# Optimization experiments

Hardware: AMD Instinct MI355X
Metric: run time of the kernel (lower is better)

The kernel has to match this reference:

```python
import jax, jax.numpy as jnp
from jax import lax
import numpy as np

D_MODEL = 96; D_STATE = 16; SSM_RATIO = 2.0; D_CONV = 3; K = 4
D_INNER = int(SSM_RATIO * D_MODEL)      # 192
DT_RANK = -(-D_MODEL // 16)             # ceil(96/16) = 6
B_SZ = 4; H = 32; W = 32

# ---- zig-zag (snake) index helpers (static numpy) ----
def _snake_h(Hh, Ww):
    idx = np.tile(np.arange(Ww), (Hh, 1)); idx[1::2] = idx[1::2, ::-1]; return idx  # (H,W)

def _snake_v(Hh, Ww):
    idx = np.tile(np.arange(Hh)[:, None], (1, Ww)); idx[:, 1::2] = idx[::-1, 1::2]; return idx  # (H,W)

def _h_scan(x, d):
    Hh, Ww = x.shape[-2:]
    if d == 'left':
        x = jnp.flip(x, (-1, -2))
    return x[:, :, np.arange(Hh)[:, None], _snake_h(Hh, Ww)]

def _v_scan(x, d):
    Bb, Cc, Hh, Ww = x.shape
    if d == 'up':
        x = jnp.flip(x, (-1, -2))
    t = x[:, :, _snake_v(Hh, Ww), np.arange(Ww)[None, :]]  # gather along H per column
    return jnp.swapaxes(t, -1, -2).reshape(Bb, Cc, Hh, Ww)

def _h_merge(x, d):
    Hh, Ww = x.shape[-2:]
    t = x[:, :, np.arange(Hh)[:, None], _snake_h(Hh, Ww)]
    if d == 'left':
        t = jnp.flip(t, (-1, -2))
    return t

def _v_merge(x, d):
    Hh, Ww = x.shape[-2:]
    t2 = jnp.swapaxes(x, -1, -2)  # (B,C,W,H); requires H==W like the torch source
    t = t2[:, :, _snake_v(Hh, Ww), np.arange(Ww)[None, :]]
    if d == 'up':
        t = jnp.flip(t, (-1, -2))
    return t

def cross_scan(x):
    return jnp.stack([_v_scan(x, 'down'), _v_scan(x, 'up'), _h_scan(x, 'right'), _h_scan(x, 'left')], axis=1)

def cross_merge(ys):
    return (_v_merge(ys[:, 0], 'down') + _v_merge(ys[:, 1], 'up')
            + _h_merge(ys[:, 2], 'right') + _h_merge(ys[:, 3], 'left'))

def selective_scan(u, delta, A, Bs, Cs, Dp, delta_bias):
    # u,delta:(B,K,D,L)  A:(K,D,N)  Bs,Cs:(B,K,N,L)  Dp,delta_bias:(K,D)
    delta = jax.nn.softplus(delta + delta_bias[None, :, :, None])
    dA = jnp.exp(jnp.einsum('bkdl,kdn->lbkdn', delta, A))
    dBu = jnp.einsum('bkdl,bkdl,bknl->lbkdn', delta, u, Bs)
    Ct = jnp.moveaxis(Cs, -1, 0)  # (L,B,K,N)
    def step(h, inp):
        dA_t, dBu_t, c_t = inp
        h = dA_t * h + dBu_t
        return h, jnp.einsum('bkdn,bkn->bkd', h, c_t)
    h0 = jnp.zeros(dA.shape[1:], u.dtype)
    _, ys = lax.scan(step, h0, (dA, dBu, Ct))
    return jnp.moveaxis(ys, 0, -1) + Dp[None, :, :, None] * u  # (B,K,D,L)

def setup_inputs() -> dict:
    key = jax.random.key(0)
    ks = jax.random.split(key, 8)
    x = jax.random.normal(ks[0], (B_SZ, D_MODEL, H, W), jnp.float32)
    in_proj_w = jax.random.normal(ks[1], (2 * D_INNER, D_MODEL), jnp.float32) * (D_MODEL ** -0.5)
    conv_w = jax.random.normal(ks[2], (D_INNER, 1, D_CONV, D_CONV), jnp.float32) * 0.2  # depthwise
    conv_b = jnp.zeros((D_INNER,), jnp.float32)
    x_proj_w = jax.random.normal(ks[3], (K, DT_RANK + 2 * D_STATE, D_INNER), jnp.float32) * (D_INNER ** -0.5)
    s = DT_RANK ** -0.5
    dt_w = jax.random.uniform(ks[4], (K, D_INNER, DT_RANK), jnp.float32, -s, s)
    dt = jax.random.uniform(ks[5], (K, D_INNER), jnp.float32, 0.001, 0.1)
    dt_b = jnp.log(jnp.expm1(dt))  # inverse softplus, as in dt_init
    A_logs = jnp.tile(jnp.log(jnp.arange(1, D_STATE + 1, dtype=jnp.float32)), (K * D_INNER, 1))
    Ds = jnp.ones((K * D_INNER,), jnp.float32)
    gn_gamma = jnp.ones((D_INNER,), jnp.float32)
    gn_beta = jnp.zeros((D_INNER,), jnp.float32)
    out_proj_w = jax.random.normal(ks[6], (D_MODEL, D_INNER), jnp.float32) * (D_INNER ** -0.5)
    return {'x': x, 'in_proj_w': in_proj_w, 'conv_w': conv_w, 'conv_b': conv_b,
            'x_proj_w': x_proj_w, 'dt_w': dt_w, 'dt_b': dt_b, 'A_logs': A_logs, 'Ds': Ds,
            'gn_gamma': gn_gamma, 'gn_beta': gn_beta, 'out_proj_w': out_proj_w}

def reference(x, in_proj_w, conv_w, conv_b, x_proj_w, dt_w, dt_b, A_logs, Ds, gn_gamma, gn_beta, out_proj_w):
    Bb, _, Hh, Ww = x.shape; L = Hh * Ww
    xz = jnp.einsum('bchw,oc->bohw', x, in_proj_w)          # in_proj (1x1 conv, no bias)
    xx, z = jnp.split(xz, 2, axis=1)
    z = jax.nn.silu(z)
    xx = lax.conv_general_dilated(xx, conv_w, (1, 1), 'SAME', feature_group_count=D_INNER,
                                  dimension_numbers=('NCHW', 'OIHW', 'NCHW')) + conv_b[None, :, None, None]
    xx = jax.nn.silu(xx)
    xs = cross_scan(xx).reshape(Bb, K, D_INNER, L)          # 4-direction zig-zag scan
    x_dbl = jnp.einsum('bkdl,kcd->bkcl', xs, x_proj_w)
    dts = jnp.einsum('bkrl,kdr->bkdl', x_dbl[:, :, :DT_RANK], dt_w)
    Bs = x_dbl[:, :, DT_RANK:DT_RANK + D_STATE]
    Cs = x_dbl[:, :, DT_RANK + D_STATE:]
    A = -jnp.exp(A_logs).reshape(K, D_INNER, D_STATE)
    y = selective_scan(xs, dts, A, Bs, Cs, Ds.reshape(K, D_INNER), dt_b)
    y = cross_merge(y.reshape(Bb, K, D_INNER, Hh, Ww))       # (B,D,H,W)
    # out_norm: GroupNorm(1, d_inner) == layernorm over (C,H,W) per sample
    mu = jnp.mean(y, axis=(1, 2, 3), keepdims=True)
    var = jnp.var(y, axis=(1, 2, 3), keepdims=True)
    y = (y - mu) * lax.rsqrt(var + 1e-6)
    y = y * gn_gamma[None, :, None, None] + gn_beta[None, :, None, None]
    y = y * z
    return jnp.einsum('bchw,oc->bohw', y, out_proj_w)
```

## Files before the change

### kernel.cpp

```cpp
#include <hip/hip_runtime.h>
#include <math.h>

#define Bsz 4
#define DM 96
#define DI 192
#define NS 16
#define RK 6
#define KK 4
#define HH 32
#define WW 32
#define LL 1024
#define NC 64
#define CS 16

__device__ __forceinline__ float silu_f(float x) { return x / (1.f + __expf(-x)); }

__device__ __forceinline__ int l_of_hw(int k, int h, int w) {
    if (k == 1 || k == 3) { h = 31 - h; w = 31 - w; }
    if (k < 2) return w * 32 + ((w & 1) ? 31 - h : h);
    return h * 32 + ((h & 1) ? 31 - w : w);
}

__global__ void in_proj_k(const float* __restrict__ x, const float* __restrict__ w,
                          float* __restrict__ xx, float* __restrict__ zs,
                          float* __restrict__ stats) {
    int bi = blockIdx.x;
    int t = threadIdx.x;
    if (bi == 0 && t < 2 * Bsz) stats[t] = 0.f;
    int lb = bi & 3;
    int og = (bi >> 2) % 48;
    int b = bi / 192;
    int l = lb * 256 + t;
    const float* xb = x + (size_t)b * DM * LL + l;
    float acc[8];
#pragma unroll
    for (int g = 0; g < 8; g++) acc[g] = 0.f;
    for (int c = 0; c < DM; c++) {
        float xv = xb[(size_t)c * LL];
#pragma unroll
        for (int g = 0; g < 8; g++)
            acc[g] = fmaf(xv, w[(size_t)(og * 8 + g) * DM + c], acc[g]);
    }
#pragma unroll
    for (int g = 0; g < 8; g++) {
        int o = og * 8 + g;
        if (o < DI) xx[((size_t)b * DI + o) * LL + l] = acc[g];
        else        zs[((size_t)b * DI + (o - DI)) * LL + l] = silu_f(acc[g]);
    }
}

__global__ void convxs_k(const float* __restrict__ xx, const float* __restrict__ cw,
                         const float* __restrict__ cb, float* __restrict__ xs) {
    __shared__ float tile[32][65];
    int bi = blockIdx.x;
    int h0 = bi % 32;
    int dt = (bi / 32) % 3;
    int b = bi / 96;
    int d0 = dt * 64;
    int t = threadIdx.x;
    int wi = t & 31, dg = t >> 5;

#pragma unroll
    for (int pass = 0; pass < 8; pass++) {
        int di = pass * 8 + dg;
        int d = d0 + di;
        const float* xp = xx + ((size_t)b * DI + d) * LL;
        const float* wp = cw + d * 9;
        float acc = cb[d];
#pragma unroll
        for (int kh = 0; kh < 3; kh++) {
            int hh = h0 + kh - 1;
            if (hh < 0 || hh >= HH) continue;
#pragma unroll
            for (int kw = 0; kw < 3; kw++) {
                int ww2 = wi + kw - 1;
                if (ww2 < 0 || ww2 >= WW) continue;
                acc = fmaf(xp[hh * WW + ww2], wp[kh * 3 + kw], acc);
            }
        }
        tile[wi][di] = silu_f(acc);
    }
    __syncthreads();

    int di = t & 63, hg = t >> 6;
#pragma unroll
    for (int k = 0; k < KK; k++) {
        float* xsk = xs + ((size_t)b * KK + k) * LL * DI;
#pragma unroll
        for (int rep = 0; rep < 8; rep++) {
            int w2 = rep * 4 + hg;
            int l = l_of_hw(k, h0, w2);
            xsk[(size_t)l * DI + d0 + di] = tile[w2][di];
        }
    }
}

__global__ void __launch_bounds__(512)
xdbl_k(const float* __restrict__ xs, const float* __restrict__ xpw,
       float* __restrict__ xdbl) {
    __shared__ float tile[64 * 193];
    int blk = blockIdx.x;
    int bk = blk >> 4, lt = blk & 15;
    int k = bk & 3;
    int t = threadIdx.x;

    const float4* src4 = (const float4*)(xs + ((size_t)bk * LL + lt * 64) * DI);
#pragma unroll
    for (int i = 0; i < 6; i++) {
        int j4 = t + i * 512;
        float4 v = src4[j4];
        int l = j4 / 48;
        int d = (j4 % 48) * 4;
        float* dst = &tile[l * 193 + d];
        dst[0] = v.x; dst[1] = v.y; dst[2] = v.z; dst[3] = v.w;
    }
    __syncthreads();

    int ll = t & 63;
    int cg = t >> 6;
    int c0 = cg * 5;
    int wlim = (c0 + 5 <= 38) ? 5 : (38 - c0);
    const float* wk = xpw + (size_t)k * 38 * DI;

    float acc[5];
#pragma unroll
    for (int j = 0; j < 5; j++) acc[j] = 0.f;
    const float* xrow = &tile[ll * 193];
#pragma unroll 4
    for (int d = 0; d < DI; d++) {
        float xv = xrow[d];
#pragma unroll
        for (int j = 0; j < 5; j++) {
            int cc = c0 + j; cc = (cc > 37) ? 37 : cc;
            acc[j] = fmaf(xv, wk[(size_t)cc * DI + d], acc[j]);
        }
    }
    float* orow = xdbl + ((size_t)bk * LL + lt * 64 + ll) * 38;
#pragma unroll
    for (int j = 0; j < 5; j++)
        if (j < wlim) orow[c0 + j] = acc[j];
}

__global__ void scan_p1(const float* __restrict__ xs, const float* __restrict__ xdbl,
                        const float* __restrict__ dtw_g, const float* __restrict__ dtb_g,
                        const float* __restrict__ Alog,
                        float* __restrict__ Pst, float* __restrict__ Hloc) {
    int blk = blockIdx.x;
    int bk = blk / NC, c = blk % NC;
    int k = bk & 3;
    int d = threadIdx.x;
    int kd = k * DI + d;

    float A[NS];
#pragma unroll
    for (int n = 0; n < NS; n++) A[n] = -__expf(Alog[(size_t)kd * NS + n]);
    float dtw[RK];
#pragma unroll
    for (int r = 0; r < RK; r++) dtw[r] = dtw_g[(size_t)kd * RK + r];
    float dtb = dtb_g[kd];

    float h[NS], P[NS];
#pragma unroll
    for (int n = 0; n < NS; n++) { h[n] = 0.f; P[n] = 1.f; }

    const float* xdbase = xdbl + ((size_t)bk * LL + c * CS) * 38;
    const float* xsbase = xs + ((size_t)bk * LL + c * CS) * DI;

    for (int s = 0; s < CS; s++) {
        const float* xd = xdbase + s * 38;
        float dt = dtb;
#pragma unroll
        for (int r = 0; r < RK; r++) dt = fmaf(xd[r], dtw[r], dt);
        dt = (dt > 20.f) ? dt : log1pf(__expf(dt));
        float du = dt * xsbase[(size_t)s * DI + d];
#pragma unroll
        for (int n = 0; n < NS; n++) {
            float a = __expf(dt * A[n]);
            h[n] = fmaf(a, h[n], du * xd[6 + n]);
            P[n] *= a;
        }
    }
    size_t base = ((size_t)blk * DI + d) * NS;
#pragma unroll
    for (int n = 0; n < NS; n++) { Pst[base + n] = P[n]; Hloc[base + n] = h[n]; }
}

__global__ void scan_mid(const float* __restrict__ Pst, float* __restrict__ Hloc) {
    int gid = blockIdx.x * 256 + threadIdx.x;
    int bk = gid / (DI * NS);
    int dn = gid % (DI * NS);
    size_t base = (size_t)bk * NC * DI * NS + dn;
    float h = 0.f;
    for (int c = 0; c < NC; c++) {
        size_t a = base + (size_t)c * DI * NS;
        float p = Pst[a];
        float loc = Hloc[a];
        Hloc[a] = h;
        h = fmaf(p, h, loc);
    }
}

__global__ void scan_p3(const float* __restrict__ xs, const float* __restrict__ xdbl,
                        const float* __restrict__ dtw_g, const float* __restrict__ dtb_g,
                        const float* __restrict__ Alog, const float* __restrict__ Ds,
                        const float* __restrict__ Hin, float* __restrict__ ys) {
    int blk = blockIdx.x;
    int bk = blk / NC, c = blk % NC;
    int k = bk & 3;
    int d = threadIdx.x;
    int kd = k * DI + d;

    float A[NS];
#pragma unroll
    for (int n = 0; n < NS; n++) A[n] = -__expf(Alog[(size_t)kd * NS + n]);
    float dtw[RK];
#pragma unroll
    for (int r = 0; r < RK; r++) dtw[r] = dtw_g[(size_t)kd * RK + r];
    float dtb = dtb_g[kd];
    float Dp = Ds[kd];

    float h[NS];
    size_t hbase = ((size_t)blk * DI + d) * NS;
#pragma unroll
    for (int n = 0; n < NS; n++) h[n] = Hin[hbase + n];

    const float* xdbase = xdbl + ((size_t)bk * LL + c * CS) * 38;
    const float* xsbase = xs + ((size_t)bk * LL + c * CS) * DI;
    float* ybase = ys + ((size_t)bk * LL + c * CS) * DI;

    for (int s = 0; s < CS; s++) {
        const float* xd = xdbase + s * 38;
        float dt = dtb;
#pragma unroll
        for (int r = 0; r < RK; r++) dt = fmaf(xd[r], dtw[r], dt);
        dt = (dt > 20.f) ? dt : log1pf(__expf(dt));
        float u = xsbase[(size_t)s * DI + d];
        float du = dt * u;
        float y = 0.f;
#pragma unroll
        for (int n = 0; n < NS; n++) {
            float a = __expf(dt * A[n]);
            h[n] = fmaf(a, h[n], du * xd[6 + n]);
            y = fmaf(h[n], xd[22 + n], y);
        }
        ybase[(size_t)s * DI + d] = fmaf(Dp, u, y);
    }
}

#define MT 16
__global__ void merge_k(const float* __restrict__ ys, float* __restrict__ ym,
                        float* __restrict__ stats) {
    __shared__ float tile[MT][DI + 1];
    __shared__ float sh1[3], sh2[3];
    int b = blockIdx.y;
    int hw0 = blockIdx.x * MT;
    int d = threadIdx.x;
    const float* yb = ys + (size_t)b * KK * LL * DI;

    float s1 = 0.f, s2 = 0.f;
#pragma unroll
    for (int hwi = 0; hwi < MT; hwi++) {
        int hw = hw0 + hwi;
        int h = hw >> 5, w = hw & 31;
        int l0 = l_of_hw(0, h, w);
        int l1 = l_of_hw(1, h, w);
        int l2 = l_of_hw(2, h, w);
        int l3 = l_of_hw(3, h, w);
        float v = yb[((size_t)0 * LL + l0) * DI + d]
                + yb[((size_t)1 * LL + l1) * DI + d]
                + yb[((size_t)2 * LL + l2) * DI + d]
                + yb[((size_t)3 * LL + l3) * DI + d];
        tile[hwi][d] = v;
        s1 += v; s2 = fmaf(v, v, s2);
    }
#pragma unroll
    for (int off = 32; off > 0; off >>= 1) {
        s1 += __shfl_down(s1, off);
        s2 += __shfl_down(s2, off);
    }
    int lane = threadIdx.x & 63, wid = threadIdx.x >> 6;
    if (lane == 0) { sh1[wid] = s1; sh2[wid] = s2; }
    __syncthreads();
    if (threadIdx.x == 0) {
        atomicAdd(&stats[b * 2],     sh1[0] + sh1[1] + sh1[2]);
        atomicAdd(&stats[b * 2 + 1], sh2[0] + sh2[1] + sh2[2]);
    }
#pragma unroll
    for (int rep = 0; rep < MT; rep++) {
        int j = rep * DI + threadIdx.x;
        int d2 = j >> 4;
        int hwi = j & (MT - 1);
        ym[((size_t)b * DI + d2) * LL + hw0 + hwi] = tile[hwi][d2];
    }
}

__global__ void yz_k(const float* __restrict__ ym, const float* __restrict__ zs,
                     const float* __restrict__ g, const float* __restrict__ be,
                     const float* __restrict__ stats, float* __restrict__ yz) {
    int idx = blockIdx.x * 256 + threadIdx.x;
    int c = (idx >> 10) % DI;
    int b = idx / (LL * DI);
    const float Ninv = 1.f / (float)(DI * LL);
    float mu = stats[b * 2] * Ninv;
    float var = stats[b * 2 + 1] * Ninv - mu * mu;
    float rstd = rsqrtf(var + 1e-6f);
    float v = (ym[idx] - mu) * rstd * g[c] + be[c];
    yz[idx] = v * zs[idx];
}

__global__ void out_k(const float* __restrict__ yz, const float* __restrict__ wo,
                      float* __restrict__ out) {
    int bi = blockIdx.x;
    int t = threadIdx.x;
    int lb = bi & 3;
    int og = (bi >> 2) % 24;
    int b = bi / 96;
    int l = lb * 256 + t;
    const float* yb = yz + (size_t)b * DI * LL + l;
    float acc[4];
#pragma unroll
    for (int g = 0; g < 4; g++) acc[g] = 0.f;
    for (int c = 0; c < DI; c++) {
        float yv = yb[(size_t)c * LL];
#pragma unroll
        for (int g = 0; g < 4; g++)
            acc[g] = fmaf(yv, wo[(size_t)(og * 4 + g) * DI + c], acc[g]);
    }
#pragma unroll
    for (int g = 0; g < 4; g++)
        out[((size_t)b * DM + og * 4 + g) * LL + l] = acc[g];
}

extern "C" void kernel_launch(void* const* d_in, const int* in_sizes, int n_in,
                              void* d_out, int out_size, void* d_ws, size_t ws_size,
                              hipStream_t stream) {
    const float* x    = (const float*)d_in[0];
    const float* ipw  = (const float*)d_in[1];
    const float* cw   = (const float*)d_in[2];
    const float* cb   = (const float*)d_in[3];
    const float* xpw  = (const float*)d_in[4];
    const float* dtw  = (const float*)d_in[5];
    const float* dtb  = (const float*)d_in[6];
    const float* Alog = (const float*)d_in[7];
    const float* Ds   = (const float*)d_in[8];
    const float* gng  = (const float*)d_in[9];
    const float* gnb  = (const float*)d_in[10];
    const float* opw  = (const float*)d_in[11];
    float* out = (float*)d_out;

    float* ws = (float*)d_ws;
    const size_t o_xx   = 0;
    const size_t o_zs   = o_xx + (size_t)Bsz * DI * LL;
    const size_t o_xs   = o_zs + (size_t)Bsz * DI * LL;
    const size_t o_xdbl = o_xs + (size_t)Bsz * KK * LL * DI;
    const size_t o_P    = o_xdbl + (size_t)Bsz * KK * LL * 38;
    const size_t o_H    = o_P + (size_t)Bsz * KK * NC * DI * NS;
    const size_t o_st   = o_H + (size_t)Bsz * KK * NC * DI * NS;

    float* xx    = ws + o_xx;
    float* zs    = ws + o_zs;
    float* xs    = ws + o_xs;
    float* xdbl  = ws + o_xdbl;
    float* Pst   = ws + o_P;
    float* Hst   = ws + o_H;
    float* stats = ws + o_st;
    float* ys = Pst;
    float* ym = xx;
    float* yz = Hst;

    hipLaunchKernelGGL(in_proj_k, dim3(768), dim3(256), 0, stream, x, ipw, xx, zs, stats);
    hipLaunchKernelGGL(convxs_k, dim3(384), dim3(256), 0, stream, xx, cw, cb, xs);
    hipLaunchKernelGGL(xdbl_k, dim3(256), dim3(512), 0, stream, xs, xpw, xdbl);
    hipLaunchKernelGGL(scan_p1, dim3(Bsz * KK * NC), dim3(192), 0, stream,
                       xs, xdbl, dtw, dtb, Alog, Pst, Hst);
    hipLaunchKernelGGL(scan_mid, dim3(192), dim3(256), 0, stream, Pst, Hst);
    hipLaunchKernelGGL(scan_p3, dim3(Bsz * KK * NC), dim3(192), 0, stream,
                       xs, xdbl, dtw, dtb, Alog, Ds, Hst, ys);
    hipLaunchKernelGGL(merge_k, dim3(LL / MT, Bsz), dim3(192), 0, stream, ys, ym, stats);
    hipLaunchKernelGGL(yz_k, dim3(3072), dim3(256), 0, stream, ym, zs, gng, gnb, stats, yz);
    hipLaunchKernelGGL(out_k, dim3(384), dim3(256), 0, stream, yz, opw, out);
}
```

Before: 233.9 us.

## Store conv output once in HW order and gather scan directions by index

The conv kernel now writes one transposed (L,D) copy of the activations instead of four direction-permuted copies. The xdbl and scan kernels gather rows through a snake-index mapping, and scan_p3 writes outputs in spatial order so the merge reads contiguously. It also halves the chunk count for the chunked scan, vectorises and prefetches scan_mid, and uses a fast log for softplus. This cuts global writes and reads of the 4x replicated tensor, but the scan has half as many blocks (less parallelism) and slightly less accurate softplus.

```diff
diff --git a/kernel.cpp b/kernel.cpp
--- a/kernel.cpp
+++ b/kernel.cpp
@@ -10,15 +10,19 @@
 #define HH 32
 #define WW 32
 #define LL 1024
-#define NC 64
-#define CS 16
+#define NC 32
+#define CS 32
 
 __device__ __forceinline__ float silu_f(float x) { return x / (1.f + __expf(-x)); }
 
-__device__ __forceinline__ int l_of_hw(int k, int h, int w) {
-    if (k == 1 || k == 3) { h = 31 - h; w = 31 - w; }
-    if (k < 2) return w * 32 + ((w & 1) ? 31 - h : h);
-    return h * 32 + ((h & 1) ? 31 - w : w);
+__device__ __forceinline__ int hw_of_l(int k, int l) {
+    int a = l >> 5, r = l & 31;
+    int m = (a & 1) ? 31 - r : r;
+    int h, w;
+    if (k < 2) { w = a; h = m; }
+    else       { h = a; w = m; }
+    if (k & 1) { h = 31 - h; w = 31 - w; }
+    return h * 32 + w;
 }
 
 __global__ void in_proj_k(const float* __restrict__ x, const float* __restrict__ w,
@@ -49,8 +53,8 @@
     }
 }
 
-__global__ void convxs_k(const float* __restrict__ xx, const float* __restrict__ cw,
-                         const float* __restrict__ cb, float* __restrict__ xs) {
+__global__ void convT_k(const float* __restrict__ xx, const float* __restrict__ cw,
+                        const float* __restrict__ cb, float* __restrict__ xxT) {
     __shared__ float tile[32][65];
     int bi = blockIdx.x;
     int h0 = bi % 32;
@@ -82,36 +86,32 @@
     }
     __syncthreads();
 
-    int di = t & 63, hg = t >> 6;
-#pragma unroll
-    for (int k = 0; k < KK; k++) {
-        float* xsk = xs + ((size_t)b * KK + k) * LL * DI;
-#pragma unroll
-        for (int rep = 0; rep < 8; rep++) {
-            int w2 = rep * 4 + hg;
-            int l = l_of_hw(k, h0, w2);
-            xsk[(size_t)l * DI + d0 + di] = tile[w2][di];
-        }
+    int di = t & 63, w4 = t >> 6;
+#pragma unroll
+    for (int rep = 0; rep < 8; rep++) {
+        int w2 = rep * 4 + w4;
+        xxT[((size_t)b * LL + h0 * 32 + w2) * DI + d0 + di] = tile[w2][di];
     }
 }
 
 __global__ void __launch_bounds__(512)
-xdbl_k(const float* __restrict__ xs, const float* __restrict__ xpw,
+xdbl_k(const float* __restrict__ xxT, const float* __restrict__ xpw,
        float* __restrict__ xdbl) {
     __shared__ float tile[64 * 193];
     int blk = blockIdx.x;
     int bk = blk >> 4, lt = blk & 15;
-    int k = bk & 3;
+    int k = bk & 3, b = bk >> 2;
     int t = threadIdx.x;
 
-    const float4* src4 = (const float4*)(xs + ((size_t)bk * LL + lt * 64) * DI);
+    const float* xb = xxT + (size_t)b * LL * DI;
 #pragma unroll
     for (int i = 0; i < 6; i++) {
         int j4 = t + i * 512;
-        float4 v = src4[j4];
-        int l = j4 / 48;
-        int d = (j4 % 48) * 4;
-        float* dst = &tile[l * 193 + d];
+        int lr = j4 / 48;
+        int d4 = j4 % 48;
+        int hw = hw_of_l(k, lt * 64 + lr);
+        float4 v = ((const float4*)(xb + (size_t)hw * DI))[d4];
+        float* dst = &tile[lr * 193 + d4 * 4];
         dst[0] = v.x; dst[1] = v.y; dst[2] = v.z; dst[3] = v.w;
     }
     __syncthreads();
@@ -141,13 +141,13 @@
         if (j < wlim) orow[c0 + j] = acc[j];
 }
 
-__global__ void scan_p1(const float* __restrict__ xs, const float* __restrict__ xdbl,
+__global__ void scan_p1(const float* __restrict__ xxT, const float* __restrict__ xdbl,
                         const float* __restrict__ dtw_g, const float* __restrict__ dtb_g,
                         const float* __restrict__ Alog,
                         float* __restrict__ Pst, float* __restrict__ Hloc) {
     int blk = blockIdx.x;
     int bk = blk / NC, c = blk % NC;
-    int k = bk & 3;
+    int k = bk & 3, b = bk >> 2;
     int d = threadIdx.x;
     int kd = k * DI + d;
 
@@ -164,15 +164,17 @@
     for (int n = 0; n < NS; n++) { h[n] = 0.f; P[n] = 1.f; }
 
     const float* xdbase = xdbl + ((size_t)bk * LL + c * CS) * 38;
-    const float* xsbase = xs + ((size_t)bk * LL + c * CS) * DI;
+    const float* xb = xxT + (size_t)b * LL * DI;
 
     for (int s = 0; s < CS; s++) {
         const float* xd = xdbase + s * 38;
+        int hw = hw_of_l(k, c * CS + s);
+        float u = xb[(size_t)hw * DI + d];
         float dt = dtb;
 #pragma unroll
         for (int r = 0; r < RK; r++) dt = fmaf(xd[r], dtw[r], dt);
-        dt = (dt > 20.f) ? dt : log1pf(__expf(dt));
-        float du = dt * xsbase[(size_t)s * DI + d];
+        dt = (dt > 20.f) ? dt : __logf(1.f + __expf(dt));
+        float du = dt * u;
 #pragma unroll
         for (int n = 0; n < NS; n++) {
             float a = __expf(dt * A[n]);
@@ -187,26 +189,43 @@
 
 __global__ void scan_mid(const float* __restrict__ Pst, float* __restrict__ Hloc) {
     int gid = blockIdx.x * 256 + threadIdx.x;
-    int bk = gid / (DI * NS);
-    int dn = gid % (DI * NS);
-    size_t base = (size_t)bk * NC * DI * NS + dn;
-    float h = 0.f;
-    for (int c = 0; c < NC; c++) {
-        size_t a = base + (size_t)c * DI * NS;
-        float p = Pst[a];
-        float loc = Hloc[a];
-        Hloc[a] = h;
-        h = fmaf(p, h, loc);
-    }
-}
-
-__global__ void scan_p3(const float* __restrict__ xs, const float* __restrict__ xdbl,
+    int bk = gid / 1536;
+    int j = gid % 1536;
+    const float2* Pp = (const float2*)(Pst + (size_t)bk * NC * (DI * NS)) + j;
+    float2* Hp = (float2*)(Hloc + (size_t)bk * NC * (DI * NS)) + j;
+    const int S = (DI * NS) / 2;
+
+    float2 h = make_float2(0.f, 0.f);
+    float2 P[4], L[4];
+#pragma unroll
+    for (int q = 0; q < 4; q++) { P[q] = Pp[(size_t)q * S]; L[q] = Hp[(size_t)q * S]; }
+    for (int c = 0; c < NC; c += 4) {
+        float2 Pn[4], Ln[4];
+        if (c + 4 < NC) {
+#pragma unroll
+            for (int q = 0; q < 4; q++) {
+                Pn[q] = Pp[(size_t)(c + 4 + q) * S];
+                Ln[q] = Hp[(size_t)(c + 4 + q) * S];
+            }
+        }
+#pragma unroll
+        for (int q = 0; q < 4; q++) {
+            Hp[(size_t)(c + q) * S] = h;
+            h.x = fmaf(P[q].x, h.x, L[q].x);
+            h.y = fmaf(P[q].y, h.y, L[q].y);
+        }
+#pragma unroll
+        for (int q = 0; q < 4; q++) { P[q] = Pn[q]; L[q] = Ln[q]; }
+    }
+}
+
+__global__ void scan_p3(const float* __restrict__ xxT, const float* __restrict__ xdbl,
                         const float* __restrict__ dtw_g, const float* __restrict__ dtb_g,
                         const float* __restrict__ Alog, const float* __restrict__ Ds,
-                        const float* __restrict__ Hin, float* __restrict__ ys) {
+                        const float* __restrict__ Hin, float* __restrict__ ysm) {
     int blk = blockIdx.x;
     int bk = blk / NC, c = blk % NC;
-    int k = bk & 3;
+    int k = bk & 3, b = bk >> 2;
     int d = threadIdx.x;
     int kd = k * DI + d;
 
@@ -225,16 +244,17 @@
     for (int n = 0; n < NS; n++) h[n] = Hin[hbase + n];
 
     const float* xdbase = xdbl + ((size_t)bk * LL + c * CS) * 38;
-    const float* xsbase = xs + ((size_t)bk * LL + c * CS) * DI;
-    float* ybase = ys + ((size_t)bk * LL + c * CS) * DI;
+    const float* xb = xxT + (size_t)b * LL * DI;
+    float* yk = ysm + (size_t)bk * LL * DI;
 
     for (int s = 0; s < CS; s++) {
         const float* xd = xdbase + s * 38;
+        int hw = hw_of_l(k, c * CS + s);
+        float u = xb[(size_t)hw * DI + d];
         float dt = dtb;
 #pragma unroll
         for (int r = 0; r < RK; r++) dt = fmaf(xd[r], dtw[r], dt);
-        dt = (dt > 20.f) ? dt : log1pf(__expf(dt));
-        float u = xsbase[(size_t)s * DI + d];
+        dt = (dt > 20.f) ? dt : __logf(1.f + __expf(dt));
         float du = dt * u;
         float y = 0.f;
 #pragma unroll
@@ -243,33 +263,28 @@
             h[n] = fmaf(a, h[n], du * xd[6 + n]);
             y = fmaf(h[n], xd[22 + n], y);
         }
-        ybase[(size_t)s * DI + d] = fmaf(Dp, u, y);
+        yk[(size_t)hw * DI + d] = fmaf(Dp, u, y);
     }
 }
 
 #define MT 16
-__global__ void merge_k(const float* __restrict__ ys, float* __restrict__ ym,
+__global__ void merge_k(const float* __restrict__ ysm, float* __restrict__ ym,
                         float* __restrict__ stats) {
     __shared__ float tile[MT][DI + 1];
     __shared__ float sh1[3], sh2[3];
     int b = blockIdx.y;
     int hw0 = blockIdx.x * MT;
     int d = threadIdx.x;
-    const float* yb = ys + (size_t)b * KK * LL * DI;
+    const float* yb = ysm + (size_t)b * KK * LL * DI;
 
     float s1 = 0.f, s2 = 0.f;
 #pragma unroll
     for (int hwi = 0; hwi < MT; hwi++) {
         int hw = hw0 + hwi;
-        int h = hw >> 5, w = hw & 31;
-        int l0 = l_of_hw(0, h, w);
-        int l1 = l_of_hw(1, h, w);
-        int l2 = l_of_hw(2, h, w);
-        int l3 = l_of_hw(3, h, w);
-        float v = yb[((size_t)0 * LL + l0) * DI + d]
-                + yb[((size_t)1 * LL + l1) * DI + d]
-                + yb[((size_t)2 * LL + l2) * DI + d]
-                + yb[((size_t)3 * LL + l3) * DI + d];
+        float v = yb[((size_t)0 * LL + hw) * DI + d]
+                + yb[((size_t)1 * LL + hw) * DI + d]
+                + yb[((size_t)2 * LL + hw) * DI + d]
+                + yb[((size_t)3 * LL + hw) * DI + d];
         tile[hwi][d] = v;
         s1 += v; s2 = fmaf(v, v, s2);
     }
@@ -350,33 +365,34 @@
 
     float* ws = (float*)d_ws;
     const size_t o_xx   = 0;
-    const size_t o_zs   = o_xx + (size_t)Bsz * DI * LL;
-    const size_t o_xs   = o_zs + (size_t)Bsz * DI * LL;
-    const size_t o_xdbl = o_xs + (size_t)Bsz * KK * LL * DI;
+    const size_t o_zs   = o_xx   + (size_t)Bsz * DI * LL;
+    const size_t o_xxT  = o_zs   + (size_t)Bsz * DI * LL;
+    const size_t o_xdbl = o_xxT  + (size_t)Bsz * LL * DI;
     const size_t o_P    = o_xdbl + (size_t)Bsz * KK * LL * 38;
-    const size_t o_H    = o_P + (size_t)Bsz * KK * NC * DI * NS;
-    const size_t o_st   = o_H + (size_t)Bsz * KK * NC * DI * NS;
+    const size_t o_H    = o_P    + (size_t)Bsz * KK * NC * DI * NS;
+    const size_t o_ysm  = o_H    + (size_t)Bsz * KK * NC * DI * NS;
+    const size_t o_st   = o_ysm  + (size_t)Bsz * KK * LL * DI;
 
     float* xx    = ws + o_xx;
     float* zs    = ws + o_zs;
-    float* xs    = ws + o_xs;
+    float* xxT   = ws + o_xxT;
     float* xdbl  = ws + o_xdbl;
     float* Pst   = ws + o_P;
     float* Hst   = ws + o_H;
+    float* ysm   = ws + o_ysm;
     float* stats = ws + o_st;
-    float* ys = Pst;
     float* ym = xx;
-    float* yz = Hst;
+    float* yz = Pst;
 
     hipLaunchKernelGGL(in_proj_k, dim3(768), dim3(256), 0, stream, x, ipw, xx, zs, stats);
-    hipLaunchKernelGGL(convxs_k, dim3(384), dim3(256), 0, stream, xx, cw, cb, xs);
-    hipLaunchKernelGGL(xdbl_k, dim3(256), dim3(512), 0, stream, xs, xpw, xdbl);
+    hipLaunchKernelGGL(convT_k, dim3(384), dim3(256), 0, stream, xx, cw, cb, xxT);
+    hipLaunchKernelGGL(xdbl_k, dim3(256), dim3(512), 0, stream, xxT, xpw, xdbl);
     hipLaunchKernelGGL(scan_p1, dim3(Bsz * KK * NC), dim3(192), 0, stream,
-                       xs, xdbl, dtw, dtb, Alog, Pst, Hst);
-    hipLaunchKernelGGL(scan_mid, dim3(192), dim3(256), 0, stream, Pst, Hst);
+                       xxT, xdbl, dtw, dtb, Alog, Pst, Hst);
+    hipLaunchKernelGGL(scan_mid, dim3(96), dim3(256), 0, stream, Pst, Hst);
     hipLaunchKernelGGL(scan_p3, dim3(Bsz * KK * NC), dim3(192), 0, stream,
-                       xs, xdbl, dtw, dtb, Alog, Ds, Hst, ys);
-    hipLaunchKernelGGL(merge_k, dim3(LL / MT, Bsz), dim3(192), 0, stream, ys, ym, stats);
+                       xxT, xdbl, dtw, dtb, Alog, Ds, Hst, ysm);
+    hipLaunchKernelGGL(merge_k, dim3(LL / MT, Bsz), dim3(192), 0, stream, ysm, ym, stats);
     hipLaunchKernelGGL(yz_k, dim3(3072), dim3(256), 0, stream, ym, zs, gng, gnb, stats, yz);
     hipLaunchKernelGGL(out_k, dim3(384), dim3(256), 0, stream, yz, opw, out);
 }
```

Measured after the change: 211.8 us. -9.5%, faster.
